# Kernel tuning notes

Hardware: AMD Instinct MI355X
Metric: run time of the kernel (lower is better)

## Reference

```python
import jax, jax.numpy as jnp
import numpy as np

B, N, F, H = 2, 2048, 1024, 16
HD = F // H
SQRT_D = float(np.sqrt(F))  # note: module scales by sqrt(in_c), not sqrt(head_dim)


def setup_inputs() -> dict:
    key = jax.random.key(0)
    ks = jax.random.split(key, 9)
    s = 1.0 / np.sqrt(F)
    mk = lambda k: jax.random.uniform(k, (F, F), jnp.float32, -s, s)
    mb = lambda k: jax.random.uniform(k, (F,), jnp.float32, -s, s)
    return {
        "x": jax.random.normal(ks[0], (B, N, F), jnp.float32),
        "Wq": mk(ks[1]), "bq": mb(ks[2]),
        "Wk": mk(ks[3]), "bk": mb(ks[4]),
        "Wv": mk(ks[5]), "bv": mb(ks[6]),
        "Wo": mk(ks[7]), "bo": mb(ks[8]),
    }


def reference(x, Wq, bq, Wk, bk, Wv, bv, Wo, bo):
    b, n, f = x.shape
    # projections (torch Linear: x @ W.T + b); view to (b, n, h, hd)
    q = (x @ Wq.T + bq).reshape(b, n, H, HD)
    k = (x @ Wk.T + bk).reshape(b, n, H, HD)
    v = (x @ Wv.T + bv).reshape(b, n, H, HD)
    score = jnp.einsum('bihd,bjhd->bhij', q, k)
    attn = jax.nn.softmax(score / SQRT_D, axis=-1)
    o = jnp.einsum('bhij,bjhd->bihd', attn, v).reshape(b, n, f)
    return o @ Wo.T + bo
```

## Files before the change

kernel.cpp:

```cpp
#include <hip/hip_runtime.h>
#include <hip/hip_bf16.h>
#include <stdint.h>
#include <stddef.h>

typedef __bf16 bf16;
typedef __attribute__((ext_vector_type(8))) __bf16 bf16x8;
typedef __attribute__((ext_vector_type(4))) __bf16 bf16x4;
typedef __attribute__((ext_vector_type(2))) __bf16 bf16x2;
typedef __attribute__((ext_vector_type(4))) float f32x4;

#define MFMA16(a, b, c) __builtin_amdgcn_mfma_f32_16x16x32_bf16(a, b, c, 0, 0, 0)

#define BB 2
#define SEQ 2048
#define FDIM 1024
#define NH 16
#define HD 64
#define M_TOK 4096
#define N_QKV 3072

#define CSC 0.04508422f

__device__ __forceinline__ void gll16(const bf16* g, bf16* l) {
    __builtin_amdgcn_global_load_lds(
        (const __attribute__((address_space(1))) void*)g,
        (__attribute__((address_space(3))) void*)l, 16, 0, 0);
}

__device__ __forceinline__ bf16 pack_bf16(float f) {
    uint32_t u = __builtin_bit_cast(uint32_t, f);
    uint16_t h = (uint16_t)((u + 0x8000u) >> 16);
    return __builtin_bit_cast(bf16, h);
}

__device__ __forceinline__ uint32_t pk2(float a, float b) {
#if __has_builtin(__builtin_amdgcn_cvt_pk_bf16_f32)
    bf16x2 t = __builtin_amdgcn_cvt_pk_bf16_f32(a, b);
    return __builtin_bit_cast(uint32_t, t);
#else
    uint32_t ua = __builtin_bit_cast(uint32_t, a) + 0x8000u;
    uint32_t ub = __builtin_bit_cast(uint32_t, b) + 0x8000u;
    return __builtin_amdgcn_perm(ub, ua, 0x07060302);
#endif
}

__global__ __launch_bounds__(256) void convert_k(
    const float* __restrict__ x,
    const float* __restrict__ Wq, const float* __restrict__ bq,
    const float* __restrict__ Wk, const float* __restrict__ bk,
    const float* __restrict__ Wv, const float* __restrict__ bv,
    const float* __restrict__ Wo,
    bf16* __restrict__ xb, bf16* __restrict__ Wcat, bf16* __restrict__ Wob,
    float* __restrict__ bcat)
{
    const int tid = blockIdx.x * blockDim.x + threadIdx.x;
    const int nt = gridDim.x * blockDim.x;
    const int NX4 = M_TOK * FDIM / 4;
    const int NW4 = FDIM * FDIM / 4;

    for (int i = tid; i < NX4; i += nt) {
        float4 v = ((const float4*)x)[i];
        bf16x4 o; o[0] = (bf16)v.x; o[1] = (bf16)v.y; o[2] = (bf16)v.z; o[3] = (bf16)v.w;
        ((bf16x4*)xb)[i] = o;
    }
    for (int i = tid; i < NW4; i += nt) {
        float4 v = ((const float4*)Wq)[i];
        bf16x4 o;
        o[0] = (bf16)(v.x * CSC); o[1] = (bf16)(v.y * CSC);
        o[2] = (bf16)(v.z * CSC); o[3] = (bf16)(v.w * CSC);
        ((bf16x4*)Wcat)[i] = o;
        v = ((const float4*)Wk)[i];
        o[0] = (bf16)v.x; o[1] = (bf16)v.y; o[2] = (bf16)v.z; o[3] = (bf16)v.w;
        ((bf16x4*)Wcat)[NW4 + i] = o;
        v = ((const float4*)Wv)[i];
        o[0] = (bf16)v.x; o[1] = (bf16)v.y; o[2] = (bf16)v.z; o[3] = (bf16)v.w;
        ((bf16x4*)Wcat)[2 * NW4 + i] = o;
        v = ((const float4*)Wo)[i];
        o[0] = (bf16)v.x; o[1] = (bf16)v.y; o[2] = (bf16)v.z; o[3] = (bf16)v.w;
        ((bf16x4*)Wob)[i] = o;
    }
    for (int i = tid; i < FDIM; i += nt) {
        bcat[i] = bq[i] * CSC;
        bcat[FDIM + i] = bk[i];
        bcat[2 * FDIM + i] = bv[i];
    }
}

__global__ __launch_bounds__(512, 2) void gemm256(
    const bf16* __restrict__ A,
    const bf16* __restrict__ Bw,
    const float* __restrict__ bias,
    bf16* __restrict__ Cb,
    bf16* __restrict__ VtOut,
    int M, int N, int K)
{
    extern __shared__ char smem[];
    const int tid = threadIdx.x;
    const int lane = tid & 63;
    const int wave = tid >> 6;
    const int wr = wave >> 2;
    const int wc = wave & 3;
    const int m0 = blockIdx.y * 256;
    const int n0 = blockIdx.x * 256;
    const int lrow = lane & 15;
    const int quad = lane >> 4;
    const int NT = K >> 6;

    const int l8 = lane >> 3;
    const int kx = ((lane & 7) ^ l8) << 3;
    const int lcl = wave * 16 + l8;

#define ASTG(sl, kt, mh, c) do { \
    const int _lc = lcl + (c) * 8; \
    const int _gr = m0 + ((_lc >> 6) << 7) + ((mh) << 6) + (_lc & 63); \
    gll16(A + (size_t)_gr * K + (size_t)(kt) * 64 + kx, \
          (bf16*)(smem + (sl) * 65536 + (mh) * 16384 + wave * 2048 + (c) * 1024)); \
} while (0)
#define BSTG(sl, kt, nh, c) do { \
    const int _lc = lcl + (c) * 8; \
    const int _gc = n0 + ((_lc >> 5) << 6) + ((nh) << 5) + (_lc & 31); \
    gll16(Bw + (size_t)_gc * K + (size_t)(kt) * 64 + kx, \
          (bf16*)(smem + (sl) * 65536 + 32768 + (nh) * 16384 + wave * 2048 + (c) * 1024)); \
} while (0)

    const int swz0 = ((quad ^ (lrow & 7)) << 4);
    const int swz1 = (((4 + quad) ^ (lrow & 7)) << 4);
    const int arow = (wr * 64 + lrow) * 128;
    const int brow = (wc * 32 + lrow) * 128;

    f32x4 acc[8][4] = {};
    bf16x8 af[4][2];
    bf16x8 bc[2][2][2];

    ASTG(0, 0, 0, 0); ASTG(0, 0, 0, 1);
    BSTG(0, 0, 0, 0); BSTG(0, 0, 0, 1);
    BSTG(0, 0, 1, 0); BSTG(0, 0, 1, 1);
    ASTG(0, 0, 1, 0); ASTG(0, 0, 1, 1);
    asm volatile("s_waitcnt vmcnt(4)" ::: "memory");
    __builtin_amdgcn_s_barrier();

    for (int t = 0; t < NT; ++t) {
        const int sl = t & 1;
        const int ns = sl ^ 1;
        const char* sb = smem + sl * 65536;
        const bool pf = (t + 1 < NT);

#pragma unroll
        for (int ph = 0; ph < 4; ++ph) {
            const int mh = ph >> 1, nh = ph & 1;
            if (pf) {
                if (ph == 0)      { ASTG(ns, t + 1, 0, 0); ASTG(ns, t + 1, 0, 1); }
                else if (ph == 1) { BSTG(ns, t + 1, 0, 0); BSTG(ns, t + 1, 0, 1); }
                else if (ph == 2) { BSTG(ns, t + 1, 1, 0); BSTG(ns, t + 1, 1, 1); }
                else              { ASTG(ns, t + 1, 1, 0); ASTG(ns, t + 1, 1, 1); }
            }
            if (nh == 0) {
#pragma unroll
                for (int iq = 0; iq < 4; ++iq) {
                    af[iq][0] = *(const bf16x8*)(sb + mh * 16384 + arow + iq * 2048 + swz0);
                    af[iq][1] = *(const bf16x8*)(sb + mh * 16384 + arow + iq * 2048 + swz1);
                }
            }
            if (ph == 0 || ph == 1) {
#pragma unroll
                for (int jq = 0; jq < 2; ++jq) {
                    bc[nh][jq][0] = *(const bf16x8*)(sb + 32768 + nh * 16384 + brow + jq * 2048 + swz0);
                    bc[nh][jq][1] = *(const bf16x8*)(sb + 32768 + nh * 16384 + brow + jq * 2048 + swz1);
                }
            }
            __builtin_amdgcn_s_setprio(1);
#pragma unroll
            for (int iq = 0; iq < 4; ++iq)
#pragma unroll
                for (int jq = 0; jq < 2; ++jq) {
                    acc[mh * 4 + iq][nh * 2 + jq] =
                        MFMA16(af[iq][0], bc[nh][jq][0], acc[mh * 4 + iq][nh * 2 + jq]);
                    acc[mh * 4 + iq][nh * 2 + jq] =
                        MFMA16(af[iq][1], bc[nh][jq][1], acc[mh * 4 + iq][nh * 2 + jq]);
                }
            __builtin_amdgcn_s_setprio(0);
            if (pf) asm volatile("s_waitcnt vmcnt(4)" ::: "memory");
            else    asm volatile("s_waitcnt vmcnt(0)" ::: "memory");
            __builtin_amdgcn_s_barrier();
        }
    }
#undef ASTG
#undef BSTG

    if (VtOut && n0 >= 2048) {
        const int bql = (m0 >> 11);
#pragma unroll
        for (int i = 0; i < 8; ++i) {
#pragma unroll
            for (int j = 0; j < 4; ++j) {
                const int col = n0 + wc * 64 + (j >> 1) * 32 + (j & 1) * 16 + lrow;
                const float bsv = bias[col];
                const int vh = col - 2048;
                const int row = m0 + wr * 128 + (i >> 2) * 64 + (i & 3) * 16 + quad * 4;
                const int jj = row & (SEQ - 1);
                const int g = jj & 63;
                const int jj2 = (jj & ~63) | ((g >> 5) << 5)
                              | (((g >> 2) & 3) << 3) | (((g >> 4) & 1) << 2);
                bf16x4 vv;
#pragma unroll
                for (int r = 0; r < 4; ++r)
                    vv[r] = pack_bf16(acc[i][j][r] + bsv);
                *(bf16x4*)&VtOut[((size_t)bql * 16 * 64 + vh) * SEQ + jj2] = vv;
            }
        }
        return;
    }
#pragma unroll
    for (int i = 0; i < 8; ++i) {
#pragma unroll
        for (int j = 0; j < 4; ++j) {
            const int col = n0 + wc * 64 + (j >> 1) * 32 + (j & 1) * 16 + lrow;
            const float bsv = bias[col];
#pragma unroll
            for (int r = 0; r < 4; ++r) {
                const int row = m0 + wr * 128 + (i >> 2) * 64 + (i & 3) * 16 + quad * 4 + r;
                Cb[(size_t)row * N + col] = pack_bf16(acc[i][j][r] + bsv);
            }
        }
    }
}

template<int MT>
__global__ __launch_bounds__(256) void gemm_bt(
    const bf16* __restrict__ A,
    const bf16* __restrict__ Bw,
    const float* __restrict__ bias,
    float* __restrict__ Cf,
    int M, int N, int K)
{
    constexpr int RI = MT / 32;
    __shared__ __align__(16) bf16 As[2][MT * 32];
    __shared__ __align__(16) bf16 Bs[2][128 * 32];

    const int tid = threadIdx.x;
    const int lane = tid & 63;
    const int wave = tid >> 6;
    const int m0 = blockIdx.y * MT;
    const int n0 = blockIdx.x * 128;
    const int wm = (wave >> 1) * (MT / 2);
    const int wn = (wave & 1) * 64;
    const int lrow = lane & 15;
    const int quad = lane >> 4;

    f32x4 acc[RI][4] = {};

    const int srow = wave * 16 + (lane >> 2);
    const int scol = ((lane & 3) ^ ((lane >> 3) & 3)) * 8;
    const bf16* Ag = A + (size_t)(m0 + srow) * K + scol;
    const bf16* Bg = Bw + (size_t)(n0 + srow) * K + scol;
    const int wo = (wave * 16) * 32;
    const int swz8 = (quad ^ ((lrow >> 1) & 3)) * 8;

    gll16(Ag, &As[0][wo]);
    if (MT == 128) gll16(Ag + (size_t)64 * K, &As[0][wo + 2048]);
    gll16(Bg, &Bs[0][wo]);
    gll16(Bg + (size_t)64 * K, &Bs[0][wo + 2048]);

    for (int k0 = 0, it = 0; k0 < K; k0 += 32, ++it) {
        const int cur = it & 1;
        __syncthreads();

        if (k0 + 32 < K) {
            const int nxt = cur ^ 1;
            gll16(Ag + k0 + 32, &As[nxt][wo]);
            if (MT == 128) gll16(Ag + (size_t)64 * K + k0 + 32, &As[nxt][wo + 2048]);
            gll16(Bg + k0 + 32, &Bs[nxt][wo]);
            gll16(Bg + (size_t)64 * K + k0 + 32, &Bs[nxt][wo + 2048]);
        }

        bf16x8 af[RI], bfr[4];
#pragma unroll
        for (int s = 0; s < RI; ++s)
            af[s] = *(const bf16x8*)&As[cur][(wm + s * 16 + lrow) * 32 + swz8];
#pragma unroll
        for (int s = 0; s < 4; ++s)
            bfr[s] = *(const bf16x8*)&Bs[cur][(wn + s * 16 + lrow) * 32 + swz8];
#pragma unroll
        for (int i = 0; i < RI; ++i)
#pragma unroll
            for (int j = 0; j < 4; ++j)
                acc[i][j] = MFMA16(af[i], bfr[j], acc[i][j]);
    }

    const int r0 = quad * 4;
#pragma unroll
    for (int i = 0; i < RI; ++i) {
#pragma unroll
        for (int j = 0; j < 4; ++j) {
            const int col = n0 + wn + j * 16 + lrow;
            const float bsv = bias[col];
#pragma unroll
            for (int r = 0; r < 4; ++r) {
                const int row = m0 + wm + i * 16 + r0 + r;
                Cf[(size_t)row * N + col] = acc[i][j][r] + bsv;
            }
        }
    }
}

__global__ __launch_bounds__(512, 4) void attn_k(
    const bf16* __restrict__ QKV,
    const bf16* __restrict__ Vt,
    bf16* __restrict__ O)
{
    const int bx = blockIdx.x;
    const int bh = (bx & 7) + 8 * ((bx >> 3) & 3);
    const int qblk = bx >> 5;
    const int b = bh >> 4;
    const int h = bh & 15;
    const int lane = threadIdx.x & 63;
    const int wave = threadIdx.x >> 6;
    const int qg = wave & 3;
    const int jp = wave >> 2;
    const int lrow = lane & 15;
    const int quad = lane >> 4;
    const int lk8 = quad * 8;

    __shared__ __align__(16) bf16 Ks[2][2][128 * 32];
    __shared__ __align__(16) bf16 Vs[2][4][64 * 32];

    const size_t base = (size_t)b * SEQ * N_QKV;
    const bf16* Qp = QKV + base + h * HD;
    const bf16* Kp = QKV + base + FDIM + h * HD;
    const bf16* Vtp = Vt + (size_t)bh * HD * SEQ;

    const int qr0 = qblk * 128 + qg * 32;

    bf16x8 qf[2][2];
#pragma unroll
    for (int qt = 0; qt < 2; ++qt)
#pragma unroll
        for (int ks = 0; ks < 2; ++ks)
            qf[qt][ks] = *(const bf16x8*)(Qp + (size_t)(qr0 + qt * 16 + lrow) * N_QKV
                                          + ks * 32 + lk8);

    bf16x8 ones8;
#pragma unroll
    for (int e = 0; e < 8; ++e) ones8[e] = (bf16)1.0f;

    const f32x4 zf = {0.f, 0.f, 0.f, 0.f};

    f32x4 o[2][4] = {};
    f32x4 o4[2] = {};

    const int srow = wave * 16 + (lane >> 2);
    const int scol = ((lane & 3) ^ ((lane >> 3) & 3)) * 8;
    const bf16* kg = Kp + (size_t)srow * N_QKV + scol;
    const int vsrow = qg * 16 + (lane >> 2);
    const bf16* vg = Vtp + (size_t)vsrow * SEQ + jp * 32 + scol;
    const int kwo = wave * 512;
    const int swz8 = (quad ^ ((lrow >> 1) & 3)) * 8;

    gll16(kg,      &Ks[0][0][0] + kwo);
    gll16(kg + 32, &Ks[0][1][0] + kwo);
    gll16(vg,      &Vs[0][0][0] + kwo);
    gll16(vg + 64, &Vs[0][2][0] + kwo);
    kg += (size_t)128 * N_QKV;
    vg += 128;

    for (int jt = 0; jt < SEQ / 128; ++jt) {
        const int cur = jt & 1;
        __syncthreads();

        if (jt + 1 < SEQ / 128) {
            const int nxt = cur ^ 1;
            gll16(kg,      &Ks[nxt][0][0] + kwo);
            gll16(kg + 32, &Ks[nxt][1][0] + kwo);
            gll16(vg,      &Vs[nxt][0][0] + kwo);
            gll16(vg + 64, &Vs[nxt][2][0] + kwo);
            kg += (size_t)128 * N_QKV;
            vg += 128;
        }

#pragma unroll
        for (int pp = 0; pp < 2; ++pp) {
            const int p = (pp << 1) | jp;
            f32x4 Sp[2][2];
            __builtin_amdgcn_s_setprio(1);
#pragma unroll
            for (int m = 0; m < 2; ++m) {
                const int jn = 2 * p + m;
                bf16x8 kb0 = *(const bf16x8*)&Ks[cur][0][(jn * 16 + lrow) * 32 + swz8];
                bf16x8 kb1 = *(const bf16x8*)&Ks[cur][1][(jn * 16 + lrow) * 32 + swz8];
                Sp[m][0] = MFMA16(kb0, qf[0][0], zf);
                Sp[m][0] = MFMA16(kb1, qf[0][1], Sp[m][0]);
                Sp[m][1] = MFMA16(kb0, qf[1][0], zf);
                Sp[m][1] = MFMA16(kb1, qf[1][1], Sp[m][1]);
            }
            __builtin_amdgcn_s_setprio(0);

            union { bf16x8 v; uint32_t d[4]; } pb[2];
#pragma unroll
            for (int qt = 0; qt < 2; ++qt) {
                const f32x4 s0 = Sp[0][qt];
                const f32x4 s1 = Sp[1][qt];
                pb[qt].d[0] = pk2(__builtin_amdgcn_exp2f(s0[0]),
                                  __builtin_amdgcn_exp2f(s0[1]));
                pb[qt].d[1] = pk2(__builtin_amdgcn_exp2f(s0[2]),
                                  __builtin_amdgcn_exp2f(s0[3]));
                pb[qt].d[2] = pk2(__builtin_amdgcn_exp2f(s1[0]),
                                  __builtin_amdgcn_exp2f(s1[1]));
                pb[qt].d[3] = pk2(__builtin_amdgcn_exp2f(s1[2]),
                                  __builtin_amdgcn_exp2f(s1[3]));
            }

            __builtin_amdgcn_s_setprio(1);
            o4[0] = MFMA16(ones8, pb[0].v, o4[0]);
            o4[1] = MFMA16(ones8, pb[1].v, o4[1]);
#pragma unroll
            for (int df = 0; df < 4; ++df) {
                bf16x8 vA = *(const bf16x8*)&Vs[cur][p][(df * 16 + lrow) * 32 + swz8];
                o[0][df] = MFMA16(vA, pb[0].v, o[0][df]);
                o[1][df] = MFMA16(vA, pb[1].v, o[1][df]);
            }
            __builtin_amdgcn_s_setprio(0);
        }
    }

    __syncthreads();
    float* shO = (float*)Ks;
    float* shS = (float*)Vs;
    if (jp == 1) {
#pragma unroll
        for (int qt = 0; qt < 2; ++qt)
#pragma unroll
            for (int df = 0; df < 4; ++df)
                *(f32x4*)&shO[((((qt * 4 + df) * 4) + qg) * 64 + lane) * 4] = o[qt][df];
        shS[(qg * 64 + lane) * 2 + 0] = o4[0][0];
        shS[(qg * 64 + lane) * 2 + 1] = o4[1][0];
    }
    __syncthreads();
    if (jp == 1) return;

#pragma unroll
    for (int qt = 0; qt < 2; ++qt)
#pragma unroll
        for (int df = 0; df < 4; ++df) {
            f32x4 t = *(const f32x4*)&shO[((((qt * 4 + df) * 4) + qg) * 64 + lane) * 4];
            o[qt][df][0] += t[0]; o[qt][df][1] += t[1];
            o[qt][df][2] += t[2]; o[qt][df][3] += t[3];
        }
    const float den0 = o4[0][0] + shS[(qg * 64 + lane) * 2 + 0];
    const float den1 = o4[1][0] + shS[(qg * 64 + lane) * 2 + 1];

#pragma unroll
    for (int qt = 0; qt < 2; ++qt) {
        const float inv = 1.0f / (qt ? den1 : den0);
        const int q = qr0 + qt * 16 + lrow;
#pragma unroll
        for (int df = 0; df < 4; ++df) {
            bf16x4 vv;
#pragma unroll
            for (int r = 0; r < 4; ++r)
                vv[r] = pack_bf16(o[qt][df][r] * inv);
            *(bf16x4*)&O[(size_t)(b * SEQ + q) * FDIM + h * HD + df * 16 + quad * 4] = vv;
        }
    }
}

extern "C" void kernel_launch(void* const* d_in, const int* in_sizes, int n_in,
                              void* d_out, int out_size, void* d_ws, size_t ws_size,
                              hipStream_t stream) {
    (void)in_sizes; (void)n_in; (void)out_size; (void)ws_size;
    const float* x  = (const float*)d_in[0];
    const float* Wq = (const float*)d_in[1];
    const float* bq = (const float*)d_in[2];
    const float* Wk = (const float*)d_in[3];
    const float* bk = (const float*)d_in[4];
    const float* Wv = (const float*)d_in[5];
    const float* bv = (const float*)d_in[6];
    const float* Wo = (const float*)d_in[7];
    const float* bo = (const float*)d_in[8];
    float* out = (float*)d_out;

    char* ws = (char*)d_ws;
    bf16* xb    = (bf16*)(ws);
    bf16* Wcat  = (bf16*)(ws + 8388608);
    bf16* Wob   = (bf16*)(ws + 14680064);
    float* bcat = (float*)(ws + 16777216);
    bf16* QKV   = (bf16*)(ws + 16789504);
    bf16* Vt    = (bf16*)(ws + 41955328);
    bf16* Ob    = xb;

    static bool s_attr_done = false;
    if (!s_attr_done) {
        (void)hipFuncSetAttribute(reinterpret_cast<const void*>(gemm256),
                                  hipFuncAttributeMaxDynamicSharedMemorySize,
                                  131072);
        s_attr_done = true;
    }

    convert_k<<<dim3(1024), dim3(256), 0, stream>>>(x, Wq, bq, Wk, bk, Wv, bv, Wo,
                                                    xb, Wcat, Wob, bcat);
    gemm256<<<dim3(N_QKV / 256, M_TOK / 256), dim3(512), 131072, stream>>>(
        xb, Wcat, bcat, QKV, Vt, M_TOK, N_QKV, FDIM);
    attn_k<<<dim3((SEQ / 128) * BB * NH), dim3(512), 0, stream>>>(QKV, Vt, Ob);
    gemm_bt<128><<<dim3(FDIM / 128, M_TOK / 128), dim3(256), 0, stream>>>(
        Ob, Wob, bo, out, M_TOK, FDIM, FDIM);
}
```

Measured before the change: 187.8 us.

## Replace output projection GEMM with 8-wave K=64 pipelined kernel

Replaces the 256-thread output-projection GEMM (BK=32, 4 waves) with a 512-thread kernel that stages K=64 tiles into XOR-swizzled dynamic shared memory. Loads are split into B and A halves issued at different points of the loop, with explicit vmcnt waits and raw barriers, and s_setprio is raised around the MFMA bursts. The goal is to overlap global-to-LDS loads with compute and halve the number of loop iterations and barriers. In exchange it uses more LDS per block (64 KB) and depends on hand-counted waitcnt values being exactly right.

```diff
diff --git a/kernel.cpp b/kernel.cpp
--- a/kernel.cpp
+++ b/kernel.cpp
@@ -225,79 +225,115 @@
     }
 }
 
-template<int MT>
-__global__ __launch_bounds__(256) void gemm_bt(
+__global__ __launch_bounds__(512, 2) void gemm128(
     const bf16* __restrict__ A,
     const bf16* __restrict__ Bw,
     const float* __restrict__ bias,
     float* __restrict__ Cf,
     int M, int N, int K)
 {
-    constexpr int RI = MT / 32;
-    __shared__ __align__(16) bf16 As[2][MT * 32];
-    __shared__ __align__(16) bf16 Bs[2][128 * 32];
-
+    extern __shared__ char smem[];
     const int tid = threadIdx.x;
     const int lane = tid & 63;
     const int wave = tid >> 6;
-    const int m0 = blockIdx.y * MT;
+    const int wr = wave >> 2;
+    const int wc = wave & 3;
+    const int m0 = blockIdx.y * 128;
     const int n0 = blockIdx.x * 128;
-    const int wm = (wave >> 1) * (MT / 2);
-    const int wn = (wave & 1) * 64;
     const int lrow = lane & 15;
     const int quad = lane >> 4;
-
-    f32x4 acc[RI][4] = {};
-
-    const int srow = wave * 16 + (lane >> 2);
-    const int scol = ((lane & 3) ^ ((lane >> 3) & 3)) * 8;
-    const bf16* Ag = A + (size_t)(m0 + srow) * K + scol;
-    const bf16* Bg = Bw + (size_t)(n0 + srow) * K + scol;
-    const int wo = (wave * 16) * 32;
-    const int swz8 = (quad ^ ((lrow >> 1) & 3)) * 8;
-
-    gll16(Ag, &As[0][wo]);
-    if (MT == 128) gll16(Ag + (size_t)64 * K, &As[0][wo + 2048]);
-    gll16(Bg, &Bs[0][wo]);
-    gll16(Bg + (size_t)64 * K, &Bs[0][wo + 2048]);
-
-    for (int k0 = 0, it = 0; k0 < K; k0 += 32, ++it) {
-        const int cur = it & 1;
-        __syncthreads();
-
-        if (k0 + 32 < K) {
-            const int nxt = cur ^ 1;
-            gll16(Ag + k0 + 32, &As[nxt][wo]);
-            if (MT == 128) gll16(Ag + (size_t)64 * K + k0 + 32, &As[nxt][wo + 2048]);
-            gll16(Bg + k0 + 32, &Bs[nxt][wo]);
-            gll16(Bg + (size_t)64 * K + k0 + 32, &Bs[nxt][wo + 2048]);
-        }
-
-        bf16x8 af[RI], bfr[4];
-#pragma unroll
-        for (int s = 0; s < RI; ++s)
-            af[s] = *(const bf16x8*)&As[cur][(wm + s * 16 + lrow) * 32 + swz8];
-#pragma unroll
-        for (int s = 0; s < 4; ++s)
-            bfr[s] = *(const bf16x8*)&Bs[cur][(wn + s * 16 + lrow) * 32 + swz8];
-#pragma unroll
-        for (int i = 0; i < RI; ++i)
-#pragma unroll
-            for (int j = 0; j < 4; ++j)
-                acc[i][j] = MFMA16(af[i], bfr[j], acc[i][j]);
-    }
-
-    const int r0 = quad * 4;
-#pragma unroll
-    for (int i = 0; i < RI; ++i) {
-#pragma unroll
-        for (int j = 0; j < 4; ++j) {
-            const int col = n0 + wn + j * 16 + lrow;
+    const int NT = K >> 6;
+
+    const int l8 = lane >> 3;
+    const int kx = ((lane & 7) ^ l8) << 3;
+
+#define ASTG(sl, kt, c) do { \
+    const int _gr = m0 + (c) * 64 + wave * 8 + l8; \
+    gll16(A + (size_t)_gr * K + (size_t)(kt) * 64 + kx, \
+          (bf16*)(smem + (sl) * 32768 + (c) * 8192 + wave * 1024)); \
+} while (0)
+#define BSTG(sl, kt, c) do { \
+    const int _gc = n0 + (c) * 64 + wave * 8 + l8; \
+    gll16(Bw + (size_t)_gc * K + (size_t)(kt) * 64 + kx, \
+          (bf16*)(smem + (sl) * 32768 + 16384 + (c) * 8192 + wave * 1024)); \
+} while (0)
+
+    const int swz0 = ((quad ^ (lrow & 7)) << 4);
+    const int swz1 = (((4 + quad) ^ (lrow & 7)) << 4);
+    const int arow0 = (wr * 32 + lrow) * 128;
+    const int brow = (wc * 32 + lrow) * 128;
+
+    f32x4 acc[4][2] = {};
+    bf16x8 bfr[2][2];
+
+    BSTG(0, 0, 0); BSTG(0, 0, 1);
+    ASTG(0, 0, 0); ASTG(0, 0, 1);
+    asm volatile("s_waitcnt vmcnt(1)" ::: "memory");
+    __builtin_amdgcn_s_barrier();
+
+    for (int t = 0; t < NT; ++t) {
+        const int sl = t & 1;
+        const int ns = sl ^ 1;
+        const char* sb = smem + sl * 32768;
+        const bool pf = (t + 1 < NT);
+
+        if (pf) { BSTG(ns, t + 1, 0); BSTG(ns, t + 1, 1); }
+        bf16x8 af[2][2];
+#pragma unroll
+        for (int jq = 0; jq < 2; ++jq) {
+            bfr[jq][0] = *(const bf16x8*)(sb + 16384 + brow + jq * 2048 + swz0);
+            bfr[jq][1] = *(const bf16x8*)(sb + 16384 + brow + jq * 2048 + swz1);
+        }
+#pragma unroll
+        for (int iq = 0; iq < 2; ++iq) {
+            af[iq][0] = *(const bf16x8*)(sb + arow0 + iq * 2048 + swz0);
+            af[iq][1] = *(const bf16x8*)(sb + arow0 + iq * 2048 + swz1);
+        }
+        __builtin_amdgcn_s_setprio(1);
+#pragma unroll
+        for (int iq = 0; iq < 2; ++iq)
+#pragma unroll
+            for (int jq = 0; jq < 2; ++jq) {
+                acc[iq][jq] = MFMA16(af[iq][0], bfr[jq][0], acc[iq][jq]);
+                acc[iq][jq] = MFMA16(af[iq][1], bfr[jq][1], acc[iq][jq]);
+            }
+        __builtin_amdgcn_s_setprio(0);
+        if (pf) asm volatile("s_waitcnt vmcnt(2)" ::: "memory");
+        else    asm volatile("s_waitcnt vmcnt(0)" ::: "memory");
+        __builtin_amdgcn_s_barrier();
+
+        if (pf) { ASTG(ns, t + 1, 0); ASTG(ns, t + 1, 1); }
+#pragma unroll
+        for (int iq = 0; iq < 2; ++iq) {
+            af[iq][0] = *(const bf16x8*)(sb + 8192 + arow0 + iq * 2048 + swz0);
+            af[iq][1] = *(const bf16x8*)(sb + 8192 + arow0 + iq * 2048 + swz1);
+        }
+        __builtin_amdgcn_s_setprio(1);
+#pragma unroll
+        for (int iq = 0; iq < 2; ++iq)
+#pragma unroll
+            for (int jq = 0; jq < 2; ++jq) {
+                acc[2 + iq][jq] = MFMA16(af[iq][0], bfr[jq][0], acc[2 + iq][jq]);
+                acc[2 + iq][jq] = MFMA16(af[iq][1], bfr[jq][1], acc[2 + iq][jq]);
+            }
+        __builtin_amdgcn_s_setprio(0);
+        if (pf) asm volatile("s_waitcnt vmcnt(1)" ::: "memory");
+        else    asm volatile("s_waitcnt vmcnt(0)" ::: "memory");
+        __builtin_amdgcn_s_barrier();
+    }
+#undef ASTG
+#undef BSTG
+
+#pragma unroll
+    for (int iq = 0; iq < 4; ++iq) {
+#pragma unroll
+        for (int jq = 0; jq < 2; ++jq) {
+            const int col = n0 + wc * 32 + jq * 16 + lrow;
             const float bsv = bias[col];
 #pragma unroll
             for (int r = 0; r < 4; ++r) {
-                const int row = m0 + wm + i * 16 + r0 + r;
-                Cf[(size_t)row * N + col] = acc[i][j][r] + bsv;
+                const int row = m0 + (iq >> 1) * 64 + wr * 32 + (iq & 1) * 16 + quad * 4 + r;
+                Cf[(size_t)row * N + col] = acc[iq][jq][r] + bsv;
             }
         }
     }
@@ -492,6 +528,9 @@
         (void)hipFuncSetAttribute(reinterpret_cast<const void*>(gemm256),
                                   hipFuncAttributeMaxDynamicSharedMemorySize,
                                   131072);
+        (void)hipFuncSetAttribute(reinterpret_cast<const void*>(gemm128),
+                                  hipFuncAttributeMaxDynamicSharedMemorySize,
+                                  65536);
         s_attr_done = true;
     }
 
@@ -500,6 +539,6 @@
     gemm256<<<dim3(N_QKV / 256, M_TOK / 256), dim3(512), 131072, stream>>>(
         xb, Wcat, bcat, QKV, Vt, M_TOK, N_QKV, FDIM);
     attn_k<<<dim3((SEQ / 128) * BB * NH), dim3(512), 0, stream>>>(QKV, Vt, Ob);
-    gemm_bt<128><<<dim3(FDIM / 128, M_TOK / 128), dim3(256), 0, stream>>>(
+    gemm128<<<dim3(FDIM / 128, M_TOK / 128), dim3(512), 65536, stream>>>(
         Ob, Wob, bo, out, M_TOK, FDIM, FDIM);
 }
```

Result: faster. 184.0 us (-2.0%).
